# Performance work log

Hardware: AMD Instinct MI355X
Metric: run time of the kernel (lower is better)

Reference implementation:

```python
import jax, jax.numpy as jnp
import numpy as np

# dims: N batch, I input ch, R recurrent ch, A attention ch, HEADS, O out ch, HxW spatial
N, I, R, A, HEADS, O, H, W = 8, 128, 256, 256, 8, 256, 36, 36
HC = A // HEADS  # head channels


def _conv(x, w, pad):
    # NCHW conv, stride 1
    return jax.lax.conv_general_dilated(x, w, (1, 1), pad,
                                        dimension_numbers=('NCHW', 'OIHW', 'NCHW'))


def setup_inputs() -> dict:
    key = jax.random.key(0)
    ks = jax.random.split(key, 16)

    def wgt(k, shape):
        fan_in = int(np.prod(shape[1:]))
        return jax.random.normal(k, shape, jnp.float32) * (1.0 / float(np.sqrt(fan_in)))

    # gate biases: [init_input=-1 | init_forget=1 | 0 | 0] per CvtLstm init
    b_g = jnp.concatenate([jnp.full((R,), -1.0), jnp.full((R,), 1.0),
                           jnp.zeros((R,)), jnp.zeros((R,))]).astype(jnp.float32)

    return {
        'x': jax.random.normal(ks[0], (N, I, H, W), jnp.float32),
        'w_in': wgt(ks[1], (R, I, 1, 1)), 'b_in': jnp.zeros((R,), jnp.float32),
        'w_qx': wgt(ks[2], (A, R, 3, 3)), 'w_qh': wgt(ks[3], (A, R, 3, 3)),
        'w_kx': wgt(ks[4], (A, R, 3, 3)), 'w_kh': wgt(ks[5], (A, R, 3, 3)),
        'w_vx': wgt(ks[6], (A, R, 3, 3)), 'w_vh': wgt(ks[7], (A, R, 3, 3)),
        'w_ga': wgt(ks[8], (4 * R, A, 1, 1)), 'b_g': b_g,
        'w_gx': wgt(ks[9], (4 * R, R, 1, 1)), 'w_gh': wgt(ks[10], (4 * R, R, 1, 1)),
        'w_out': wgt(ks[11], (O, R, 1, 1)), 'b_out': jnp.zeros((O,), jnp.float32),
    }


def reference(x, w_in, b_in, w_qx, w_qh, w_kx, w_kh, w_vx, w_vh,
              w_ga, b_g, w_gx, w_gh, w_out, b_out):
    # input accumulate: 1x1 conv + bias
    xin = _conv(x, w_in, 'SAME') + b_in[None, :, None, None]
    # first step: recurrent state is zeros (past is empty)
    h = jnp.zeros_like(xin)
    c = jnp.zeros_like(xin)
    # Q: 3x3 padded conv on x and h (accumulated); K/V: 3x3 unpadded -> smaller token set
    q = (_conv(xin, w_qx, 'SAME') + _conv(h, w_qh, 'SAME')).reshape(N, HEADS, HC, H * W)
    k4 = _conv(xin, w_kx, 'VALID') + _conv(h, w_kh, 'VALID')   # [N, A, H-2, W-2]
    D = k4.shape[2] * k4.shape[3]
    k = k4.reshape(N, HEADS, HC, D)
    v = (_conv(xin, w_vx, 'VALID') + _conv(h, w_vh, 'VALID')).reshape(N, HEADS, HC, D)
    # attention: softmax over K/V tokens (dim D)
    attn = jax.nn.softmax(jnp.einsum('nhcq,nhcd->nhqd', q, k), axis=3)  # [N,HEADS,Q,D]
    a = jnp.einsum('nhcd,nhqd->nhcq', v, attn).reshape(N, A, H, W)
    # fused i/f/g/o gate projections: 1x1 conv on a + bias + 1x1 skips on x and h
    gates = (_conv(a, w_ga, 'SAME') + b_g[None, :, None, None]
             + _conv(xin, w_gx, 'SAME') + _conv(h, w_gh, 'SAME'))
    gi, gf, gg, go = jnp.split(gates, 4, axis=1)
    c = jax.nn.sigmoid(gf) * c + jax.nn.sigmoid(gi) * jnp.tanh(gg)
    hn = jax.nn.sigmoid(go) * jnp.tanh(c)
    # output 1x1 conv (dropout p=0 -> identity)
    return _conv(hn, w_out, 'SAME') + b_out[None, :, None, None]
```

## Files before the change

kernel.cpp:

```cpp
#include <hip/hip_runtime.h>
#include <math.h>

typedef unsigned int u32;
typedef unsigned short u16;
typedef unsigned long long u64;
typedef __attribute__((ext_vector_type(8))) __bf16 bf8;
typedef __attribute__((ext_vector_type(4))) float f4;

#define MFMA(a,b,c) __builtin_amdgcn_mfma_f32_16x16x32_bf16(a,b,c,0,0,0)

#define SWC(row_, c_) ((((((c_)>>1) ^ (((row_)>>3)&1))<<1) | (((c_)&1) ^ (((row_)>>4)&1))))

static __device__ __forceinline__ u32 cvtpk(float lo, float hi) {
  u32 r; asm("v_cvt_pk_bf16_f32 %0, %1, %2" : "=v"(r) : "v"(lo), "v"(hi));
  return r;
}
static __device__ __forceinline__ u16 f2b(float x) { return (u16)cvtpk(x, 0.f); }
static __device__ __forceinline__ float sigm(float x) { return 1.f/(1.f+__expf(-x)); }


__global__ __launch_bounds__(256) void k_cvt(const float* __restrict__ in,
        u16* __restrict__ out, int n) {
  int i = blockIdx.x*256 + threadIdx.x;
  if (i < n) out[i] = f2b(in[i]);
}
__global__ __launch_bounds__(256) void k_wt3(const float* __restrict__ wq,
        const float* __restrict__ wk, const float* __restrict__ wv,
        u16* __restrict__ tq, u16* __restrict__ tk, u16* __restrict__ tv) {
  const float* w = (blockIdx.y==0)?wq:(blockIdx.y==1)?wk:wv;
  u16* wt = (blockIdx.y==0)?tq:(blockIdx.y==1)?tk:tv;
  int i = blockIdx.x*256 + threadIdx.x;
  int tap = i >> 16, mm = (i & 65535) >> 8, rr = i & 255;
  wt[i] = f2b(w[(size_t)mm*2304 + rr*9 + tap]);
}
__global__ __launch_bounds__(256) void k_wtg(const float* __restrict__ w_ga,
        const float* __restrict__ w_gx, u16* __restrict__ wg) {
  int i = blockIdx.x*256 + threadIdx.x;
  int g = i >> 17, rem = i & 131071, rr = rem >> 9, kk = rem & 511;
  int gb = (g == 0) ? 0 : (g == 1) ? 512 : 768;
  float v = (kk < 256) ? w_ga[(size_t)(gb+rr)*256 + kk]
                       : w_gx[(size_t)(gb+rr)*256 + kk - 256];
  wg[i] = f2b(v);
}

__global__ __launch_bounds__(256,2) void k_xin(const float* __restrict__ x,
        const u16* __restrict__ wb, const float* __restrict__ bias,
        u16* __restrict__ out) {
  __shared__ u16 Xs[128][40];
  __shared__ u16 Ws[128][40];
  int tid = threadIdx.x, lane = tid & 63, wid = tid >> 6;
  int li = lane & 15, gr = lane >> 4;
  int p0 = blockIdx.x*128, m0 = blockIdx.y*128, n = blockIdx.z;
  int pcol = tid & 127, rg = tid >> 7;
  int wrow = tid >> 1, wh = tid & 1;
  int p = p0 + pcol;
  const float* src = x + (size_t)n*128*1296;
  const u32* wb32 = (const u32*)wb;
  f4 z = {0.f,0.f,0.f,0.f};
  f4 acc[4][4];
  #pragma unroll
  for (int i=0;i<4;i++) { acc[i][0]=z; acc[i][1]=z; acc[i][2]=z; acc[i][3]=z; }
  int wm = (wid & 1)*64, wp = (wid >> 1)*64;
  for (int k0 = 0; k0 < 128; k0 += 32) {
    u32 rx[8];
    #pragma unroll
    for (int j = 0; j < 8; j++) {
      int rp = rg*8 + j;
      float a = 0.f, b = 0.f;
      if (p < 1296) { a = src[(size_t)(k0+2*rp)*1296+p]; b = src[(size_t)(k0+2*rp+1)*1296+p]; }
      rx[j] = cvtpk(a, b);
    }
    const u32* wsrc = wb32 + (size_t)(m0+wrow)*64 + (k0>>1) + wh*8;
    int4 rwA = *(const int4*)wsrc, rwB = *(const int4*)(wsrc+4);
    *(int4*)&Xs[pcol][SWC(pcol,2*rg)*8]   = *(int4*)&rx[0];
    *(int4*)&Xs[pcol][SWC(pcol,2*rg+1)*8] = *(int4*)&rx[4];
    *(int4*)&Ws[wrow][SWC(wrow,2*wh)*8]   = rwA;
    *(int4*)&Ws[wrow][SWC(wrow,2*wh+1)*8] = rwB;
    __syncthreads();
    bf8 af[4], bx[4];
    #pragma unroll
    for (int mt=0;mt<4;mt++) { int r = wm+mt*16+li; af[mt] = *(bf8*)&Ws[r][SWC(r,gr)*8]; }
    #pragma unroll
    for (int pt=0;pt<4;pt++) { int r = wp+pt*16+li; bx[pt] = *(bf8*)&Xs[r][SWC(r,gr)*8]; }
    #pragma unroll
    for (int mt=0;mt<4;mt++)
      #pragma unroll
      for (int pt=0;pt<4;pt++)
        acc[mt][pt] = MFMA(af[mt], bx[pt], acc[mt][pt]);
    __syncthreads();
  }
  u32* out32 = (u32*)out + (size_t)n*128*1296;
  #pragma unroll
  for (int mt=0;mt<4;mt++)
    #pragma unroll
    for (int pt=0;pt<4;pt++) {
      int mb = m0 + wm + mt*16 + gr*4;
      int pp = p0 + wp + pt*16 + li;
      if (pp < 1296) {
        out32[(size_t)(mb>>1)*1296 + pp] = cvtpk(acc[mt][pt][0]+bias[mb], acc[mt][pt][1]+bias[mb+1]);
        out32[(size_t)((mb>>1)+1)*1296 + pp] = cvtpk(acc[mt][pt][2]+bias[mb+2], acc[mt][pt][3]+bias[mb+3]);
      }
    }
}

__global__ __launch_bounds__(256,3) void k_conv3(const u16* __restrict__ xin,
        const u16* __restrict__ wq, const u16* __restrict__ wk, const u16* __restrict__ wv,
        u16* __restrict__ qb, u16* __restrict__ kb, u16* __restrict__ vb) {
  __shared__ u16 Xs[2][128][40];
  __shared__ u16 Ws[2][128][40];
  int tid = threadIdx.x, lane = tid & 63, wid = tid >> 6;
  int li = lane & 15, gr = lane >> 4;
  int kind = blockIdx.y >> 1;
  int m0 = (blockIdx.y & 1)*128;
  int n = blockIdx.z;
  int P  = (kind == 0) ? 1296 : 1156;
  int WO = (kind == 0) ? 36 : 34;
  int pad = (kind == 0) ? 1 : 0;
  int p0 = blockIdx.x*128;
  if (p0 >= P) return;
  const u16* wt = (kind==0) ? wq : (kind==1) ? wk : wv;
  const u32* src32 = (const u32*)xin + (size_t)n*128*1296;
  const u32* wt32 = (const u32*)wt;
  int pcol = tid & 127, rg = tid >> 7;
  int wrow = tid >> 1, wh = tid & 1;
  int p = p0 + pcol;
  int py = 0, px = 0;
  if (p < P) { py = p / WO; px = p % WO; }
  f4 z = {0.f,0.f,0.f,0.f};
  f4 acc[4][4];
  #pragma unroll
  for (int i=0;i<4;i++) { acc[i][0]=z; acc[i][1]=z; acc[i][2]=z; acc[i][3]=z; }
  int wm = (wid & 1)*64, wp = (wid >> 1)*64;
  u32 rx[8]; int4 rwA, rwB;

  #define LOADIT(tap_, r0_) { \
    int dy = (tap_)/3 - pad, dx = (tap_)%3 - pad; \
    int sy = py + dy, sx = px + dx; \
    bool ok = (p < P) && sy >= 0 && sy < 36 && sx >= 0 && sx < 36; \
    int soff = sy*36 + sx; \
    const u32* xs = src32 + (size_t)(((r0_)>>1) + rg*8)*1296 + soff; \
    _Pragma("unroll") \
    for (int j = 0; j < 8; j++) rx[j] = ok ? xs[(size_t)j*1296] : 0u; \
    const u32* wsrc = wt32 + ((size_t)((tap_)*256 + m0 + wrow))*128 + ((r0_)>>1) + wh*8; \
    rwA = *(const int4*)wsrc; rwB = *(const int4*)(wsrc + 4); }

  LOADIT(0, 0);
  int pb = 0;
  for (int it = 0; it < 72; it++) {
    *(int4*)&Xs[pb][pcol][SWC(pcol,2*rg)*8]   = *(int4*)&rx[0];
    *(int4*)&Xs[pb][pcol][SWC(pcol,2*rg+1)*8] = *(int4*)&rx[4];
    *(int4*)&Ws[pb][wrow][SWC(wrow,2*wh)*8]   = rwA;
    *(int4*)&Ws[pb][wrow][SWC(wrow,2*wh+1)*8] = rwB;
    __syncthreads();
    if (it < 71) {
      int nt = it + 1;
      LOADIT(nt >> 3, (nt & 7)*32);
    }
    bf8 af[4], bx[4];
    #pragma unroll
    for (int mt=0;mt<4;mt++) { int r = wm+mt*16+li; af[mt] = *(bf8*)&Ws[pb][r][SWC(r,gr)*8]; }
    #pragma unroll
    for (int pt=0;pt<4;pt++) { int r = wp+pt*16+li; bx[pt] = *(bf8*)&Xs[pb][r][SWC(r,gr)*8]; }
    #pragma unroll
    for (int mt=0;mt<4;mt++)
      #pragma unroll
      for (int pt=0;pt<4;pt++)
        acc[mt][pt] = MFMA(af[mt], bx[pt], acc[mt][pt]);
    pb ^= 1;
  }
  #undef LOADIT

  if (kind <= 1) {
    u32* dst32 = (u32*)(kind==0 ? qb : kb) + (size_t)n*128*P;
    #pragma unroll
    for (int mt=0;mt<4;mt++)
      #pragma unroll
      for (int pt=0;pt<4;pt++) {
        int mb = m0 + wm + mt*16 + gr*4;
        int pp = p0 + wp + pt*16 + li;
        if (pp < P) {
          dst32[(size_t)(mb>>1)*P + pp] = cvtpk(acc[mt][pt][0], acc[mt][pt][1]);
          dst32[(size_t)((mb>>1)+1)*P + pp] = cvtpk(acc[mt][pt][2], acc[mt][pt][3]);
        }
      }
  } else {
    #pragma unroll
    for (int mt=0;mt<4;mt++)
      #pragma unroll
      for (int pt=0;pt<4;pt++) {
        int pp = p0 + wp + pt*16 + li;
        if (pp < P) {
          #pragma unroll
          for (int j=0;j<4;j++) {
            int m = m0 + wm + mt*16 + gr*4 + j;
            vb[((size_t)n*256 + m)*1156 + pp] = f2b(acc[mt][pt][j]);
          }
        }
      }
  }
}

__global__ __launch_bounds__(256,2) void k_attn(const u16* __restrict__ qbf,
        const u16* __restrict__ kbf, const u16* __restrict__ vbf, u16* __restrict__ abf) {
  __shared__ u16 Qs[128][40];
  __shared__ u16 Ks[64][40];
  __shared__ u16 Vs[2][32][40];
  __shared__ u16 Ps[4][2][32][40];
  int tid = threadIdx.x, lane = tid & 63, wid = tid >> 6;
  int li = lane & 15, gr = lane >> 4;
  int h = blockIdx.y, n = blockIdx.z;
  int q0 = blockIdx.x*128;
  const u32* Qp32 = (const u32*)qbf + ((size_t)n*128 + h*16)*1296;
  const u32* Kp32 = (const u32*)kbf + ((size_t)n*128 + h*16)*1156;
  const u16* Vp = vbf + ((size_t)n*256 + h*32)*1156;
  #pragma unroll
  for (int j = 0; j < 8; j++) {
    int idx = tid + j*256, qq = idx >> 4, cp = idx & 15;
    int gq = q0 + qq;
    ((u32*)&Qs[qq][0])[cp] = (gq < 1296) ? Qp32[(size_t)cp*1296 + gq] : 0u;
  }
  f4 z = {0.f,0.f,0.f,0.f};
  float mx[2] = {-1e30f, -1e30f}, ls[2] = {0.f, 0.f};
  f4 accO[2][2] = {{z,z},{z,z}};
  int wq = wid*32;
  int kdd = tid >> 2, kq = tid & 3;
  __syncthreads();
  for (int d0 = 0; d0 < 1156; d0 += 64) {
    {
      u32 kk[4];
      int gd = d0 + kdd;
      #pragma unroll
      for (int i = 0; i < 4; i++)
        kk[i] = (gd < 1156) ? Kp32[(size_t)(kq*4+i)*1156 + gd] : 0u;
      *(int4*)&Ks[kdd][SWC(kdd,kq)*8] = *(int4*)&kk[0];
    }
    #pragma unroll
    for (int j = 0; j < 4; j++) {
      int idx = tid + j*256, half = idx >> 9, rem = idx & 511;
      int cc = rem >> 4, dp = rem & 15;
      int gd = d0 + half*32 + dp*2; u32 v = 0;
      if (gd < 1156) v = *(const u32*)&Vp[(size_t)cc*1156 + gd];
      ((u32*)&Vs[half][cc][0])[dp] = v;
    }
    __syncthreads();
    bf8 ak[4], bq[2];
    #pragma unroll
    for (int dt=0;dt<4;dt++) { int r = dt*16+li; ak[dt] = *(bf8*)&Ks[r][SWC(r,gr)*8]; }
    #pragma unroll
    for (int qt=0;qt<2;qt++) bq[qt] = *(bf8*)&Qs[wq + qt*16 + li][8*gr];
    f4 s[2][4];
    #pragma unroll
    for (int qt=0;qt<2;qt++)
      #pragma unroll
      for (int dt=0;dt<4;dt++)
        s[qt][dt] = MFMA(ak[dt], bq[qt], z);
    bool tail = (d0 + 64 > 1156);
    #pragma unroll
    for (int qt=0;qt<2;qt++) {
      if (tail) {
        #pragma unroll
        for (int dt=0;dt<4;dt++)
          #pragma unroll
          for (int j=0;j<4;j++)
            if (d0 + dt*16 + gr*4 + j >= 1156) s[qt][dt][j] = -1e30f;
      }
      float tm = -1e30f;
      #pragma unroll
      for (int dt=0;dt<4;dt++)
        #pragma unroll
        for (int j=0;j<4;j++) tm = fmaxf(tm, s[qt][dt][j]);
      tm = fmaxf(tm, __shfl_xor(tm, 16));
      tm = fmaxf(tm, __shfl_xor(tm, 32));
      if (__any(tm > mx[qt] + 8.f)) {
        float nm = fmaxf(mx[qt], tm);
        float corr = __expf(mx[qt] - nm);
        mx[qt] = nm;
        ls[qt] *= corr;
        accO[0][qt] *= corr; accO[1][qt] *= corr;
      }
      float rs = 0.f;
      #pragma unroll
      for (int dt=0;dt<4;dt++)
        #pragma unroll
        for (int j=0;j<4;j++) {
          float e = __expf(s[qt][dt][j] - mx[qt]);
          s[qt][dt][j] = e; rs += e;
        }
      rs += __shfl_xor(rs, 16); rs += __shfl_xor(rs, 32);
      ls[qt] += rs;
      #pragma unroll
      for (int dt=0;dt<4;dt++) {
        u32 lo_ = cvtpk(s[qt][dt][0], s[qt][dt][1]);
        u32 hi_ = cvtpk(s[qt][dt][2], s[qt][dt][3]);
        u64 pk = (u64)lo_ | ((u64)hi_ << 32);
        *(u64*)&Ps[wid][dt>>1][qt*16 + li][(dt&1)*16 + gr*4] = pk;
      }
    }
    #pragma unroll
    for (int kt=0;kt<2;kt++) {
      bf8 av0 = *(bf8*)&Vs[kt][li][8*gr];
      bf8 av1 = *(bf8*)&Vs[kt][16 + li][8*gr];
      bf8 bp0 = *(bf8*)&Ps[wid][kt][li][8*gr];
      bf8 bp1 = *(bf8*)&Ps[wid][kt][16 + li][8*gr];
      accO[0][0] = MFMA(av0, bp0, accO[0][0]);
      accO[0][1] = MFMA(av0, bp1, accO[0][1]);
      accO[1][0] = MFMA(av1, bp0, accO[1][0]);
      accO[1][1] = MFMA(av1, bp1, accO[1][1]);
    }
    __syncthreads();
  }
  u32* ab32 = (u32*)abf + (size_t)n*128*1296;
  #pragma unroll
  for (int qt=0;qt<2;qt++) {
    float inv = 1.f / ls[qt];
    #pragma unroll
    for (int mt=0;mt<2;mt++) {
      int cb = h*32 + mt*16 + gr*4;
      int gq = q0 + wq + qt*16 + li;
      if (gq < 1296) {
        ab32[(size_t)(cb>>1)*1296 + gq] = cvtpk(accO[mt][qt][0]*inv, accO[mt][qt][1]*inv);
        ab32[(size_t)((cb>>1)+1)*1296 + gq] = cvtpk(accO[mt][qt][2]*inv, accO[mt][qt][3]*inv);
      }
    }
  }
}

__global__ __launch_bounds__(256,2) void k_gates(const u16* __restrict__ abf,
        const u16* __restrict__ xin, const u16* __restrict__ wg,
        const float* __restrict__ b_g, u16* __restrict__ hn) {
  __shared__ u16 Xs[128][40];
  __shared__ u16 Wg[3][64][40];
  int tid = threadIdx.x, lane = tid & 63, wid = tid >> 6;
  int li = lane & 15, gr = lane >> 4;
  int p0 = blockIdx.x*128, m0 = blockIdx.y*64, n = blockIdx.z;
  int pcol = tid & 127, rg = tid >> 7;
  int p = p0 + pcol;
  const u32* wg32 = (const u32*)wg;
  f4 z = {0.f,0.f,0.f,0.f};
  f4 acc[3][2][4];
  #pragma unroll
  for (int g=0;g<3;g++)
    #pragma unroll
    for (int mt=0;mt<2;mt++) { acc[g][mt][0]=z; acc[g][mt][1]=z; acc[g][mt][2]=z; acc[g][mt][3]=z; }
  int wm = (wid & 1)*32, wp = (wid >> 1)*64;
  for (int k0 = 0; k0 < 512; k0 += 32) {
    const u32* src32 = (const u32*)((k0 < 256) ? abf : xin)
        + (size_t)n*128*1296 + (size_t)((k0 & 255)>>1)*1296;
    u32 rx[8];
    #pragma unroll
    for (int j = 0; j < 8; j++) {
      int rp = rg*8 + j;
      rx[j] = (p < 1296) ? src32[(size_t)rp*1296 + p] : 0u;
    }
    *(int4*)&Xs[pcol][SWC(pcol,2*rg)*8]   = *(int4*)&rx[0];
    *(int4*)&Xs[pcol][SWC(pcol,2*rg+1)*8] = *(int4*)&rx[4];
    #pragma unroll
    for (int j = 0; j < 3; j++) {
      int sid = tid + j*256;
      int rid = sid >> 2, q = sid & 3;
      int g = rid >> 6, mm = rid & 63;
      const u32* wsrc = wg32 + (size_t)g*65536 + (size_t)(m0+mm)*256 + (k0>>1) + q*4;
      int4 w4 = *(const int4*)wsrc;
      *(int4*)&Wg[g][mm][SWC(mm,q)*8] = w4;
    }
    __syncthreads();
    bf8 bx[4];
    #pragma unroll
    for (int pt=0;pt<4;pt++) { int r = wp+pt*16+li; bx[pt] = *(bf8*)&Xs[r][SWC(r,gr)*8]; }
    #pragma unroll
    for (int g=0;g<3;g++)
      #pragma unroll
      for (int mt=0;mt<2;mt++) {
        int r = wm+mt*16+li;
        bf8 af = *(bf8*)&Wg[g][r][SWC(r,gr)*8];
        #pragma unroll
        for (int pt=0;pt<4;pt++)
          acc[g][mt][pt] = MFMA(af, bx[pt], acc[g][mt][pt]);
      }
    __syncthreads();
  }
  u32* hn32 = (u32*)hn + (size_t)n*128*1296;
  #pragma unroll
  for (int mt=0;mt<2;mt++)
    #pragma unroll
    for (int pt=0;pt<4;pt++) {
      int rb = m0 + wm + mt*16 + gr*4;
      int pp = p0 + wp + pt*16 + li;
      if (pp < 1296) {
        float hv[4];
        #pragma unroll
        for (int j=0;j<4;j++) {
          float gi = acc[0][mt][pt][j] + b_g[rb+j];
          float gg = acc[1][mt][pt][j] + b_g[512 + rb+j];
          float go = acc[2][mt][pt][j] + b_g[768 + rb+j];
          hv[j] = sigm(go) * tanhf(sigm(gi) * tanhf(gg));
        }
        hn32[(size_t)(rb>>1)*1296 + pp] = cvtpk(hv[0], hv[1]);
        hn32[(size_t)((rb>>1)+1)*1296 + pp] = cvtpk(hv[2], hv[3]);
      }
    }
}

__global__ __launch_bounds__(256,2) void k_out(const u16* __restrict__ hn,
        const u16* __restrict__ wb, const float* __restrict__ bias,
        float* __restrict__ out) {
  __shared__ u16 Xs[128][40];
  __shared__ u16 Ws[128][40];
  int tid = threadIdx.x, lane = tid & 63, wid = tid >> 6;
  int li = lane & 15, gr = lane >> 4;
  int p0 = blockIdx.x*128, m0 = blockIdx.y*128, n = blockIdx.z;
  int pcol = tid & 127, rg = tid >> 7;
  int wrow = tid >> 1, wh = tid & 1;
  int p = p0 + pcol;
  const u32* src32 = (const u32*)hn + (size_t)n*128*1296;
  const u32* wb32 = (const u32*)wb;
  f4 z = {0.f,0.f,0.f,0.f};
  f4 acc[4][4];
  #pragma unroll
  for (int i=0;i<4;i++) { acc[i][0]=z; acc[i][1]=z; acc[i][2]=z; acc[i][3]=z; }
  int wm = (wid & 1)*64, wp = (wid >> 1)*64;
  for (int k0 = 0; k0 < 256; k0 += 32) {
    u32 rx[8];
    #pragma unroll
    for (int j = 0; j < 8; j++) {
      int rp = rg*8 + j;
      rx[j] = (p < 1296) ? src32[(size_t)((k0>>1) + rp)*1296 + p] : 0u;
    }
    const u32* wsrc = wb32 + (size_t)(m0+wrow)*128 + (k0>>1) + wh*8;
    int4 rwA = *(const int4*)wsrc, rwB = *(const int4*)(wsrc+4);
    *(int4*)&Xs[pcol][SWC(pcol,2*rg)*8]   = *(int4*)&rx[0];
    *(int4*)&Xs[pcol][SWC(pcol,2*rg+1)*8] = *(int4*)&rx[4];
    *(int4*)&Ws[wrow][SWC(wrow,2*wh)*8]   = rwA;
    *(int4*)&Ws[wrow][SWC(wrow,2*wh+1)*8] = rwB;
    __syncthreads();
    bf8 af[4], bx[4];
    #pragma unroll
    for (int mt=0;mt<4;mt++) { int r = wm+mt*16+li; af[mt] = *(bf8*)&Ws[r][SWC(r,gr)*8]; }
    #pragma unroll
    for (int pt=0;pt<4;pt++) { int r = wp+pt*16+li; bx[pt] = *(bf8*)&Xs[r][SWC(r,gr)*8]; }
    #pragma unroll
    for (int mt=0;mt<4;mt++)
      #pragma unroll
      for (int pt=0;pt<4;pt++)
        acc[mt][pt] = MFMA(af[mt], bx[pt], acc[mt][pt]);
    __syncthreads();
  }
  #pragma unroll
  for (int mt=0;mt<4;mt++)
    #pragma unroll
    for (int pt=0;pt<4;pt++)
      #pragma unroll
      for (int j=0;j<4;j++) {
        int m = m0 + wm + mt*16 + gr*4 + j;
        int pp = p0 + wp + pt*16 + li;
        if (pp < 1296) out[((size_t)n*256 + m)*1296 + pp] = acc[mt][pt][j] + bias[m];
      }
}

extern "C" void kernel_launch(void* const* d_in, const int* in_sizes, int n_in,
                              void* d_out, int out_size, void* d_ws, size_t ws_size,
                              hipStream_t stream) {
  const float* x     = (const float*)d_in[0];
  const float* w_in  = (const float*)d_in[1];
  const float* b_in  = (const float*)d_in[2];
  const float* w_qx  = (const float*)d_in[3];
  const float* w_kx  = (const float*)d_in[5];
  const float* w_vx  = (const float*)d_in[7];
  const float* w_ga  = (const float*)d_in[9];
  const float* b_g   = (const float*)d_in[10];
  const float* w_gx  = (const float*)d_in[11];
  const float* w_out = (const float*)d_in[13];
  const float* b_out = (const float*)d_in[14];
  float* out = (float*)d_out;

  u16* ws = (u16*)d_ws;
  size_t o = 0;
  u16* xin_bf = ws + o; o += 2654208;
  u16* qbuf   = ws + o; o += 2654208;
  u16* kbuf   = ws + o; o += 2367488;
  u16* vbuf   = ws + o; o += 2367488;
  u16* abuf   = ws + o; o += 2654208;
  u16* hnb    = ws + o; o += 2654208;
  u16* wqT    = ws + o; o += 589824;
  u16* wkT    = ws + o; o += 589824;
  u16* wvT    = ws + o; o += 589824;
  u16* wgT    = ws + o; o += 393216;
  u16* winb   = ws + o; o += 32768;
  u16* woutb  = ws + o; o += 65536;

  k_cvt<<<128, 256, 0, stream>>>(w_in, winb, 32768);
  k_cvt<<<256, 256, 0, stream>>>(w_out, woutb, 65536);
  k_wt3<<<dim3(2304,3), 256, 0, stream>>>(w_qx, w_kx, w_vx, wqT, wkT, wvT);
  k_wtg<<<1536, 256, 0, stream>>>(w_ga, w_gx, wgT);

  k_xin  <<<dim3(11,2,8), 256, 0, stream>>>(x, winb, b_in, xin_bf);
  k_conv3<<<dim3(11,6,8), 256, 0, stream>>>(xin_bf, wqT, wkT, wvT, qbuf, kbuf, vbuf);
  k_attn <<<dim3(11,8,8), 256, 0, stream>>>(qbuf, kbuf, vbuf, abuf);
  k_gates<<<dim3(11,4,8), 256, 0, stream>>>(abuf, xin_bf, wgT, b_g, hnb);
  k_out  <<<dim3(11,2,8), 256, 0, stream>>>(hnb, woutb, b_out, out);
}
```

Baseline: 222.8 us.

## Restructure 3x3 conv into single-wave 64x64 tiles with register double-buffer; merge prep kernels

The QKV 3x3 conv kernel now runs as single-wavefront blocks, each computing a 64x64 output tile. It uses a K-step of 32 channels with two register sets that ping-pong global loads against MFMA work, so no block-level barrier is needed. The Q/K/V tiles are packed into one flattened grid dimension, which avoids empty blocks and gives far more blocks to fill the GPU. The four weight-conversion launches are merged into a single prep kernel to cut launch overhead, and shared arrays get 16-byte alignment. In exchange, the smaller tiles reuse less data per load, the register footprint grows, and the XOR swizzle may not cover every LDS bank conflict.

```diff
diff --git a/kernel.cpp b/kernel.cpp
--- a/kernel.cpp
+++ b/kernel.cpp
@@ -19,35 +19,42 @@
 static __device__ __forceinline__ float sigm(float x) { return 1.f/(1.f+__expf(-x)); }
 
 
-__global__ __launch_bounds__(256) void k_cvt(const float* __restrict__ in,
-        u16* __restrict__ out, int n) {
+__global__ __launch_bounds__(256) void k_prep(const float* __restrict__ w_in,
+        const float* __restrict__ w_out,
+        const float* __restrict__ wqx, const float* __restrict__ wkx,
+        const float* __restrict__ wvx,
+        const float* __restrict__ w_ga, const float* __restrict__ w_gx,
+        u16* __restrict__ winb, u16* __restrict__ woutb,
+        u16* __restrict__ tq, u16* __restrict__ tk, u16* __restrict__ tv,
+        u16* __restrict__ wg) {
+  int task = blockIdx.y;
   int i = blockIdx.x*256 + threadIdx.x;
-  if (i < n) out[i] = f2b(in[i]);
-}
-__global__ __launch_bounds__(256) void k_wt3(const float* __restrict__ wq,
-        const float* __restrict__ wk, const float* __restrict__ wv,
-        u16* __restrict__ tq, u16* __restrict__ tk, u16* __restrict__ tv) {
-  const float* w = (blockIdx.y==0)?wq:(blockIdx.y==1)?wk:wv;
-  u16* wt = (blockIdx.y==0)?tq:(blockIdx.y==1)?tk:tv;
-  int i = blockIdx.x*256 + threadIdx.x;
-  int tap = i >> 16, mm = (i & 65535) >> 8, rr = i & 255;
-  wt[i] = f2b(w[(size_t)mm*2304 + rr*9 + tap]);
-}
-__global__ __launch_bounds__(256) void k_wtg(const float* __restrict__ w_ga,
-        const float* __restrict__ w_gx, u16* __restrict__ wg) {
-  int i = blockIdx.x*256 + threadIdx.x;
-  int g = i >> 17, rem = i & 131071, rr = rem >> 9, kk = rem & 511;
-  int gb = (g == 0) ? 0 : (g == 1) ? 512 : 768;
-  float v = (kk < 256) ? w_ga[(size_t)(gb+rr)*256 + kk]
-                       : w_gx[(size_t)(gb+rr)*256 + kk - 256];
-  wg[i] = f2b(v);
+  if (task == 0) {
+    if (i < 32768) winb[i] = f2b(w_in[i]);
+    else if (i < 98304) woutb[i - 32768] = f2b(w_out[i - 32768]);
+  } else if (task <= 3) {
+    if (i < 589824) {
+      const float* w = (task==1)?wqx:(task==2)?wkx:wvx;
+      u16* wt = (task==1)?tq:(task==2)?tk:tv;
+      int tap = i >> 16, mm = (i & 65535) >> 8, rr = i & 255;
+      wt[i] = f2b(w[(size_t)mm*2304 + rr*9 + tap]);
+    }
+  } else {
+    if (i < 393216) {
+      int g = i >> 17, rem = i & 131071, rr = rem >> 9, kk = rem & 511;
+      int gb = (g == 0) ? 0 : (g == 1) ? 512 : 768;
+      float v = (kk < 256) ? w_ga[(size_t)(gb+rr)*256 + kk]
+                           : w_gx[(size_t)(gb+rr)*256 + kk - 256];
+      wg[i] = f2b(v);
+    }
+  }
 }
 
 __global__ __launch_bounds__(256,2) void k_xin(const float* __restrict__ x,
         const u16* __restrict__ wb, const float* __restrict__ bias,
         u16* __restrict__ out) {
-  __shared__ u16 Xs[128][40];
-  __shared__ u16 Ws[128][40];
+  __shared__ alignas(16) u16 Xs[128][40];
+  __shared__ alignas(16) u16 Ws[128][40];
   int tid = threadIdx.x, lane = tid & 63, wid = tid >> 6;
   int li = lane & 15, gr = lane >> 4;
   int p0 = blockIdx.x*128, m0 = blockIdx.y*128, n = blockIdx.z;
@@ -103,72 +110,85 @@
     }
 }
 
-__global__ __launch_bounds__(256,3) void k_conv3(const u16* __restrict__ xin,
+__global__ __launch_bounds__(64,2) void k_conv3(const u16* __restrict__ xin,
         const u16* __restrict__ wq, const u16* __restrict__ wk, const u16* __restrict__ wv,
         u16* __restrict__ qb, u16* __restrict__ kb, u16* __restrict__ vb) {
-  __shared__ u16 Xs[2][128][40];
-  __shared__ u16 Ws[2][128][40];
-  int tid = threadIdx.x, lane = tid & 63, wid = tid >> 6;
+  __shared__ alignas(16) u16 Xs[2][64][32];
+  __shared__ alignas(16) u16 Wsh[2][64][32];
+  int lane = threadIdx.x;
   int li = lane & 15, gr = lane >> 4;
-  int kind = blockIdx.y >> 1;
-  int m0 = (blockIdx.y & 1)*128;
-  int n = blockIdx.z;
-  int P  = (kind == 0) ? 1296 : 1156;
-  int WO = (kind == 0) ? 36 : 34;
-  int pad = (kind == 0) ? 1 : 0;
-  int p0 = blockIdx.x*128;
-  if (p0 >= P) return;
+  int tile = blockIdx.x, m0 = blockIdx.y*64, n = blockIdx.z;
+  int kind, t0;
+  if (tile < 21)      { kind = 0; t0 = tile; }
+  else if (tile < 40) { kind = 1; t0 = tile - 21; }
+  else                { kind = 2; t0 = tile - 40; }
+  int P  = kind ? 1156 : 1296;
+  int WO = kind ? 34 : 36;
+  int p0 = t0*64;
   const u16* wt = (kind==0) ? wq : (kind==1) ? wk : wv;
   const u32* src32 = (const u32*)xin + (size_t)n*128*1296;
   const u32* wt32 = (const u32*)wt;
-  int pcol = tid & 127, rg = tid >> 7;
-  int wrow = tid >> 1, wh = tid & 1;
-  int p = p0 + pcol;
+  int p = p0 + lane;
+  bool pvld = p < P;
   int py = 0, px = 0;
-  if (p < P) { py = p / WO; px = p % WO; }
+  if (pvld) { py = p / WO; px = p % WO; }
+  int fx = (lane >> 1) & 3;
+  int fr = (li >> 1) & 3;
   f4 z = {0.f,0.f,0.f,0.f};
   f4 acc[4][4];
   #pragma unroll
   for (int i=0;i<4;i++) { acc[i][0]=z; acc[i][1]=z; acc[i][2]=z; acc[i][3]=z; }
-  int wm = (wid & 1)*64, wp = (wid >> 1)*64;
-  u32 rx[8]; int4 rwA, rwB;
-
-  #define LOADIT(tap_, r0_) { \
-    int dy = (tap_)/3 - pad, dx = (tap_)%3 - pad; \
-    int sy = py + dy, sx = px + dx; \
-    bool ok = (p < P) && sy >= 0 && sy < 36 && sx >= 0 && sx < 36; \
-    int soff = sy*36 + sx; \
-    const u32* xs = src32 + (size_t)(((r0_)>>1) + rg*8)*1296 + soff; \
+  u32 rxA[16], rxB[16];
+  int4 rwA[4], rwB[4];
+
+  #define LOADIT(it_, RX, RW) { \
+    int tap_ = (it_) >> 3, r0h_ = ((it_) & 7)*16; \
+    int sy = py + tap_/3 - (kind==0 ? 1 : 0); \
+    int sx = px + tap_%3 - (kind==0 ? 1 : 0); \
+    bool ok = pvld && sy >= 0 && sy < 36 && sx >= 0 && sx < 36; \
+    const u32* xs = src32 + (size_t)r0h_*1296 + sy*36 + sx; \
     _Pragma("unroll") \
-    for (int j = 0; j < 8; j++) rx[j] = ok ? xs[(size_t)j*1296] : 0u; \
-    const u32* wsrc = wt32 + ((size_t)((tap_)*256 + m0 + wrow))*128 + ((r0_)>>1) + wh*8; \
-    rwA = *(const int4*)wsrc; rwB = *(const int4*)(wsrc + 4); }
-
-  LOADIT(0, 0);
-  int pb = 0;
-  for (int it = 0; it < 72; it++) {
-    *(int4*)&Xs[pb][pcol][SWC(pcol,2*rg)*8]   = *(int4*)&rx[0];
-    *(int4*)&Xs[pb][pcol][SWC(pcol,2*rg+1)*8] = *(int4*)&rx[4];
-    *(int4*)&Ws[pb][wrow][SWC(wrow,2*wh)*8]   = rwA;
-    *(int4*)&Ws[pb][wrow][SWC(wrow,2*wh+1)*8] = rwB;
-    __syncthreads();
-    if (it < 71) {
-      int nt = it + 1;
-      LOADIT(nt >> 3, (nt & 7)*32);
-    }
-    bf8 af[4], bx[4];
-    #pragma unroll
-    for (int mt=0;mt<4;mt++) { int r = wm+mt*16+li; af[mt] = *(bf8*)&Ws[pb][r][SWC(r,gr)*8]; }
-    #pragma unroll
-    for (int pt=0;pt<4;pt++) { int r = wp+pt*16+li; bx[pt] = *(bf8*)&Xs[pb][r][SWC(r,gr)*8]; }
-    #pragma unroll
-    for (int mt=0;mt<4;mt++)
-      #pragma unroll
-      for (int pt=0;pt<4;pt++)
-        acc[mt][pt] = MFMA(af[mt], bx[pt], acc[mt][pt]);
-    pb ^= 1;
-  }
+    for (int j = 0; j < 16; j++) RX[j] = ok ? xs[(size_t)j*1296] : 0u; \
+    const int4* wsrc = (const int4*)(wt32 + ((size_t)(tap_*256 + m0 + lane))*128 + r0h_); \
+    _Pragma("unroll") \
+    for (int c = 0; c < 4; c++) RW[c] = wsrc[c]; }
+
+  #define WRITEIT(RX, RW, b_) { \
+    _Pragma("unroll") \
+    for (int c = 0; c < 4; c++) { \
+      *(int4*)&Xs[b_][lane][(c ^ fx)*8] = *(int4*)&RX[c*4]; \
+      *(int4*)&Wsh[b_][lane][(c ^ fx)*8] = RW[c]; \
+    } }
+
+  #define MFMAIT(b_) { \
+    bf8 af[4], bx[4]; \
+    _Pragma("unroll") \
+    for (int mt=0;mt<4;mt++) af[mt] = *(bf8*)&Wsh[b_][mt*16+li][(gr ^ fr)*8]; \
+    _Pragma("unroll") \
+    for (int pt=0;pt<4;pt++) bx[pt] = *(bf8*)&Xs[b_][pt*16+li][(gr ^ fr)*8]; \
+    _Pragma("unroll") \
+    for (int mt=0;mt<4;mt++) \
+      _Pragma("unroll") \
+      for (int pt=0;pt<4;pt++) \
+        acc[mt][pt] = MFMA(af[mt], bx[pt], acc[mt][pt]); }
+
+  LOADIT(0, rxA, rwA);
+  WRITEIT(rxA, rwA, 0);
+  LOADIT(1, rxB, rwB);
+  for (int h = 0; h < 35; h++) {
+    LOADIT(2*h+2, rxA, rwA);
+    MFMAIT(0);
+    WRITEIT(rxB, rwB, 1);
+    LOADIT(2*h+3, rxB, rwB);
+    MFMAIT(1);
+    WRITEIT(rxA, rwA, 0);
+  }
+  MFMAIT(0);
+  WRITEIT(rxB, rwB, 1);
+  MFMAIT(1);
   #undef LOADIT
+  #undef WRITEIT
+  #undef MFMAIT
 
   if (kind <= 1) {
     u32* dst32 = (u32*)(kind==0 ? qb : kb) + (size_t)n*128*P;
@@ -176,8 +196,8 @@
     for (int mt=0;mt<4;mt++)
       #pragma unroll
       for (int pt=0;pt<4;pt++) {
-        int mb = m0 + wm + mt*16 + gr*4;
-        int pp = p0 + wp + pt*16 + li;
+        int mb = m0 + mt*16 + gr*4;
+        int pp = p0 + pt*16 + li;
         if (pp < P) {
           dst32[(size_t)(mb>>1)*P + pp] = cvtpk(acc[mt][pt][0], acc[mt][pt][1]);
           dst32[(size_t)((mb>>1)+1)*P + pp] = cvtpk(acc[mt][pt][2], acc[mt][pt][3]);
@@ -188,11 +208,11 @@
     for (int mt=0;mt<4;mt++)
       #pragma unroll
       for (int pt=0;pt<4;pt++) {
-        int pp = p0 + wp + pt*16 + li;
+        int pp = p0 + pt*16 + li;
         if (pp < P) {
           #pragma unroll
           for (int j=0;j<4;j++) {
-            int m = m0 + wm + mt*16 + gr*4 + j;
+            int m = m0 + mt*16 + gr*4 + j;
             vb[((size_t)n*256 + m)*1156 + pp] = f2b(acc[mt][pt][j]);
           }
         }
@@ -202,10 +222,10 @@
 
 __global__ __launch_bounds__(256,2) void k_attn(const u16* __restrict__ qbf,
         const u16* __restrict__ kbf, const u16* __restrict__ vbf, u16* __restrict__ abf) {
-  __shared__ u16 Qs[128][40];
-  __shared__ u16 Ks[64][40];
-  __shared__ u16 Vs[2][32][40];
-  __shared__ u16 Ps[4][2][32][40];
+  __shared__ alignas(16) u16 Qs[128][40];
+  __shared__ alignas(16) u16 Ks[64][40];
+  __shared__ alignas(16) u16 Vs[2][32][40];
+  __shared__ alignas(16) u16 Ps[4][2][32][40];
   int tid = threadIdx.x, lane = tid & 63, wid = tid >> 6;
   int li = lane & 15, gr = lane >> 4;
   int h = blockIdx.y, n = blockIdx.z;
@@ -328,8 +348,8 @@
 __global__ __launch_bounds__(256,2) void k_gates(const u16* __restrict__ abf,
         const u16* __restrict__ xin, const u16* __restrict__ wg,
         const float* __restrict__ b_g, u16* __restrict__ hn) {
-  __shared__ u16 Xs[128][40];
-  __shared__ u16 Wg[3][64][40];
+  __shared__ alignas(16) u16 Xs[128][40];
+  __shared__ alignas(16) u16 Wg[3][64][40];
   int tid = threadIdx.x, lane = tid & 63, wid = tid >> 6;
   int li = lane & 15, gr = lane >> 4;
   int p0 = blockIdx.x*128, m0 = blockIdx.y*64, n = blockIdx.z;
@@ -404,8 +424,8 @@
 __global__ __launch_bounds__(256,2) void k_out(const u16* __restrict__ hn,
         const u16* __restrict__ wb, const float* __restrict__ bias,
         float* __restrict__ out) {
-  __shared__ u16 Xs[128][40];
-  __shared__ u16 Ws[128][40];
+  __shared__ alignas(16) u16 Xs[128][40];
+  __shared__ alignas(16) u16 Ws[128][40];
   int tid = threadIdx.x, lane = tid & 63, wid = tid >> 6;
   int li = lane & 15, gr = lane >> 4;
   int p0 = blockIdx.x*128, m0 = blockIdx.y*128, n = blockIdx.z;
@@ -488,13 +508,11 @@
   u16* winb   = ws + o; o += 32768;
   u16* woutb  = ws + o; o += 65536;
 
-  k_cvt<<<128, 256, 0, stream>>>(w_in, winb, 32768);
-  k_cvt<<<256, 256, 0, stream>>>(w_out, woutb, 65536);
-  k_wt3<<<dim3(2304,3), 256, 0, stream>>>(w_qx, w_kx, w_vx, wqT, wkT, wvT);
-  k_wtg<<<1536, 256, 0, stream>>>(w_ga, w_gx, wgT);
+  k_prep<<<dim3(2304,5), 256, 0, stream>>>(w_in, w_out, w_qx, w_kx, w_vx,
+                                           w_ga, w_gx, winb, woutb, wqT, wkT, wvT, wgT);
 
   k_xin  <<<dim3(11,2,8), 256, 0, stream>>>(x, winb, b_in, xin_bf);
-  k_conv3<<<dim3(11,6,8), 256, 0, stream>>>(xin_bf, wqT, wkT, wvT, qbuf, kbuf, vbuf);
+  k_conv3<<<dim3(59,4,8), 64, 0, stream>>>(xin_bf, wqT, wkT, wvT, qbuf, kbuf, vbuf);
   k_attn <<<dim3(11,8,8), 256, 0, stream>>>(qbuf, kbuf, vbuf, abuf);
   k_gates<<<dim3(11,4,8), 256, 0, stream>>>(abuf, xin_bf, wgT, b_g, hnb);
   k_out  <<<dim3(11,2,8), 256, 0, stream>>>(hnb, woutb, b_out, out);
```

After: 369.6 us. +65.9%, slower.
